# Optimization experiments

Measured on AMD Instinct MI355X. Metric: run time of the kernel, lower is better.

Reference implementation:

```python
import jax, jax.numpy as jnp
import numpy as np

NUM_ATOMS = 4_000_000
NUM_TYPES = 11

def setup_inputs() -> dict:
    key = jax.random.key(0)
    k1, k2 = jax.random.split(key)
    input_coords = jax.random.normal(k1, (3 * NUM_ATOMS,), dtype=jnp.float32)
    atom_types = jax.random.randint(k2, (NUM_ATOMS,), 0, NUM_TYPES, dtype=jnp.int64)
    return {"input_coords": input_coords, "atom_types": atom_types, "num_atom_types": NUM_TYPES}

def reference(input_coords, atom_types, num_atom_types):
    # counts per atom type  [T]
    counts = jnp.bincount(atom_types, length=num_atom_types).astype(jnp.int32)
    # exclusive prefix sum -> bucket offsets  [T]
    offsets = (jnp.cumsum(counts) - counts).astype(jnp.int32)
    # stable sort by type reproduces the C++ bucket fill order:
    # atoms of the same type keep their original relative order.
    perm = jnp.argsort(atom_types, stable=True)  # [N] source index for each output slot
    coords3 = input_coords.reshape(-1, 3)        # [N,3]
    typed_coords = coords3[perm].reshape(-1)     # [3N] type-grouped flat coords
    return typed_coords, counts, offsets
```

## Files before the change

### kernel.cpp

```cpp
#include <hip/hip_runtime.h>

#define NTYPES 11
#define BLOCK  256
#define ITEMS  16
#define CHUNK  (BLOCK * ITEMS)

__global__ __launch_bounds__(BLOCK) void hist_kernel(
    const int* __restrict__ types, int N, int B, int* __restrict__ bc) {
  __shared__ int shCnt[NTYPES];
  const int tid = threadIdx.x;
  const int b = blockIdx.x;
  if (tid < NTYPES) shCnt[tid] = 0;
  __syncthreads();

  const int run = b * CHUNK + tid * ITEMS;
  int cnt[NTYPES];
#pragma unroll
  for (int t = 0; t < NTYPES; ++t) cnt[t] = 0;

  if (run < N) {
    const int* p = types + run;
    int ty[ITEMS];
#pragma unroll
    for (int k = 0; k < ITEMS; ++k) ty[k] = __builtin_nontemporal_load(p + k);
#pragma unroll
    for (int k = 0; k < ITEMS; ++k) {
#pragma unroll
      for (int t = 0; t < NTYPES; ++t) cnt[t] += (ty[k] == t) ? 1 : 0;
    }
  }

  const int lane = tid & 63;
#pragma unroll
  for (int t = 0; t < NTYPES; ++t) {
    int v = cnt[t];
    for (int o = 32; o >= 1; o >>= 1) v += __shfl_down(v, o);
    if (lane == 0) atomicAdd(&shCnt[t], v);
  }
  __syncthreads();
  if (tid < NTYPES) bc[tid * B + b] = shCnt[tid];
}

__global__ __launch_bounds__(NTYPES * 64) void scan_kernel(
    const int* __restrict__ bc, int B, int* __restrict__ scanOut,
    int* __restrict__ offs, float* __restrict__ outTail) {
  __shared__ int totals[NTYPES];
  const int lane = threadIdx.x & 63;
  const int t = threadIdx.x >> 6;

  int carry = 0;
#pragma unroll
  for (int cchunk = 0; cchunk < 16; ++cchunk) {
    const int idx = cchunk * 64 + lane;
    const int x = (idx < B) ? bc[t * B + idx] : 0;
    int incl = x;
#pragma unroll
    for (int o = 1; o < 64; o <<= 1) {
      int v = __shfl_up(incl, o);
      if (lane >= o) incl += v;
    }
    incl += carry;
    if (idx < B) scanOut[t * B + idx] = incl - x;
    carry = __shfl(incl, 63);
    if (cchunk * 64 + 64 >= B && cchunk * 64 < B) break;
  }
  if (lane == 0) totals[t] = carry;
  __syncthreads();

  if (threadIdx.x == 0) {
    int off = 0;
    for (int u = 0; u < NTYPES; ++u) {
      const int c = totals[u];
      offs[u] = off;
      outTail[u] = (float)c;
      outTail[NTYPES + u] = (float)off;
      off += c;
    }
  }
}

__global__ __launch_bounds__(BLOCK) void scatter_kernel(
    const float* __restrict__ coords, const int* __restrict__ types,
    const int* __restrict__ scanOut, const int* __restrict__ offs, int N,
    int B, float* __restrict__ out) {
  __shared__ float shC[CHUNK * 3];
  __shared__ int wtot[NTYPES][4];
  __shared__ int shOff[NTYPES + 1];
  __shared__ int shDelta[NTYPES];

  const int tid = threadIdx.x;
  const int b = blockIdx.x;
  const int lane = tid & 63;
  const int wave = tid >> 6;
  const int run = b * CHUNK + tid * ITEMS;
  const bool active = (run < N);

  int ty[ITEMS];
  int cnt[NTYPES];
#pragma unroll
  for (int t = 0; t < NTYPES; ++t) cnt[t] = 0;
#pragma unroll
  for (int k = 0; k < ITEMS; ++k) ty[k] = -1;

  float c[ITEMS * 3];
  if (active) {
    const int* p = types + run;
#pragma unroll
    for (int k = 0; k < ITEMS; ++k) ty[k] = __builtin_nontemporal_load(p + k);
    const float* cp = coords + (size_t)run * 3;
#pragma unroll
    for (int q = 0; q < ITEMS * 3; ++q)
      c[q] = __builtin_nontemporal_load(cp + q);
#pragma unroll
    for (int k = 0; k < ITEMS; ++k) {
#pragma unroll
      for (int t = 0; t < NTYPES; ++t) cnt[t] += (ty[k] == t) ? 1 : 0;
    }
  }

  int rank[NTYPES];
#pragma unroll
  for (int t = 0; t < NTYPES; ++t) {
    int incl = cnt[t];
#pragma unroll
    for (int o = 1; o < 64; o <<= 1) {
      int v = __shfl_up(incl, o);
      if (lane >= o) incl += v;
    }
    if (lane == 63) wtot[t][wave] = incl;
    rank[t] = incl - cnt[t];
  }
  __syncthreads();

  if (tid < NTYPES) {
    int loc = 0;
    for (int u = 0; u < tid; ++u)
      loc += wtot[u][0] + wtot[u][1] + wtot[u][2] + wtot[u][3];
    shOff[tid] = loc;
    shDelta[tid] = 3 * (offs[tid] + scanOut[tid * B + b] - loc);
    if (tid == NTYPES - 1) {
      shOff[NTYPES] =
          loc + wtot[tid][0] + wtot[tid][1] + wtot[tid][2] + wtot[tid][3];
    }
  }
  __syncthreads();

#pragma unroll
  for (int t = 0; t < NTYPES; ++t) {
    int wb = 0;
#pragma unroll
    for (int w = 0; w < 3; ++w) wb += (w < wave) ? wtot[t][w] : 0;
    rank[t] += wb + shOff[t];
  }

  if (active) {
#pragma unroll
    for (int k = 0; k < ITEMS; ++k) {
      const int t0 = ty[k];
      int slot = 0;
#pragma unroll
      for (int t = 0; t < NTYPES; ++t) {
        if (t0 == t) {
          slot = rank[t];
          rank[t] += 1;
        }
      }
      shC[3 * slot + 0] = c[3 * k + 0];
      shC[3 * slot + 1] = c[3 * k + 1];
      shC[3 * slot + 2] = c[3 * k + 2];
    }
  }
  __syncthreads();

  const int total = shOff[NTYPES];
  int offr[NTYPES];
  int dlt[NTYPES];
#pragma unroll
  for (int t = 0; t < NTYPES; ++t) {
    offr[t] = shOff[t];
    dlt[t] = shDelta[t];
  }
#pragma unroll
  for (int k = 0; k < ITEMS; ++k) {
    const int s = k * BLOCK + tid;
    if (s < total) {
      int d = dlt[0];
#pragma unroll
      for (int t = 1; t < NTYPES; ++t) d = (s >= offr[t]) ? dlt[t] : d;
      const int src = 3 * s;
      out[src + d + 0] = shC[src + 0];
      out[src + d + 1] = shC[src + 1];
      out[src + d + 2] = shC[src + 2];
    }
  }
}

extern "C" void kernel_launch(void* const* d_in, const int* in_sizes, int n_in,
                              void* d_out, int out_size, void* d_ws,
                              size_t ws_size, hipStream_t stream) {
  const float* coords = (const float*)d_in[0];
  const int* types = (const int*)d_in[1];
  const int N = in_sizes[1];
  const int B = (N + CHUNK - 1) / CHUNK;

  int* bc = (int*)d_ws;
  int* scanOut = bc + NTYPES * B;
  int* offs = scanOut + NTYPES * B;
  float* out = (float*)d_out;
  float* outTail = out + (size_t)3 * N;

  hist_kernel<<<B, BLOCK, 0, stream>>>(types, N, B, bc);
  scan_kernel<<<1, NTYPES * 64, 0, stream>>>(bc, B, scanOut, offs, outTail);
  scatter_kernel<<<B, BLOCK, 0, stream>>>(coords, types, scanOut, offs, N, B,
                                          out);
}
```

Measured before the change: 164.6 us.

## Halve items per thread, vectorize type/coord loads, preload scan inputs

Cuts ITEMS from 16 to 8, doubling the block count and shrinking shared memory per block, which should raise occupancy in the scatter kernel. Type and coordinate loads become int4/float4 vector loads instead of scalar nontemporal loads. The scan kernel now loads all per-block counts into registers up front (MAXCH=32 chunks) before the serial scan, so memory latency is not exposed on every chunk. The scan works only while B fits in 32*64 blocks, and the vector loads rely on 16-byte alignment of each thread's slice.

```diff
diff --git a/kernel.cpp b/kernel.cpp
--- a/kernel.cpp
+++ b/kernel.cpp
@@ -2,8 +2,9 @@
 
 #define NTYPES 11
 #define BLOCK  256
-#define ITEMS  16
+#define ITEMS  8
 #define CHUNK  (BLOCK * ITEMS)
+#define MAXCH  32
 
 __global__ __launch_bounds__(BLOCK) void hist_kernel(
     const int* __restrict__ types, int N, int B, int* __restrict__ bc) {
@@ -19,10 +20,9 @@
   for (int t = 0; t < NTYPES; ++t) cnt[t] = 0;
 
   if (run < N) {
-    const int* p = types + run;
-    int ty[ITEMS];
-#pragma unroll
-    for (int k = 0; k < ITEMS; ++k) ty[k] = __builtin_nontemporal_load(p + k);
+    const int4* p = (const int4*)(types + run);
+    int4 a0 = p[0], a1 = p[1];
+    int ty[ITEMS] = {a0.x, a0.y, a0.z, a0.w, a1.x, a1.y, a1.z, a1.w};
 #pragma unroll
     for (int k = 0; k < ITEMS; ++k) {
 #pragma unroll
@@ -47,22 +47,29 @@
   __shared__ int totals[NTYPES];
   const int lane = threadIdx.x & 63;
   const int t = threadIdx.x >> 6;
+  const int nch = (B + 63) >> 6;
+
+  int x[MAXCH];
+#pragma unroll
+  for (int c = 0; c < MAXCH; ++c) {
+    const int idx = c * 64 + lane;
+    x[c] = (c < nch && idx < B) ? bc[t * B + idx] : 0;
+  }
 
   int carry = 0;
 #pragma unroll
-  for (int cchunk = 0; cchunk < 16; ++cchunk) {
-    const int idx = cchunk * 64 + lane;
-    const int x = (idx < B) ? bc[t * B + idx] : 0;
-    int incl = x;
+  for (int c = 0; c < MAXCH; ++c) {
+    if (c >= nch) break;
+    int incl = x[c];
 #pragma unroll
     for (int o = 1; o < 64; o <<= 1) {
       int v = __shfl_up(incl, o);
       if (lane >= o) incl += v;
     }
     incl += carry;
-    if (idx < B) scanOut[t * B + idx] = incl - x;
+    const int idx = c * 64 + lane;
+    if (idx < B) scanOut[t * B + idx] = incl - x[c];
     carry = __shfl(incl, 63);
-    if (cchunk * 64 + 64 >= B && cchunk * 64 < B) break;
   }
   if (lane == 0) totals[t] = carry;
   __syncthreads();
@@ -104,13 +111,20 @@
 
   float c[ITEMS * 3];
   if (active) {
-    const int* p = types + run;
-#pragma unroll
-    for (int k = 0; k < ITEMS; ++k) ty[k] = __builtin_nontemporal_load(p + k);
-    const float* cp = coords + (size_t)run * 3;
-#pragma unroll
-    for (int q = 0; q < ITEMS * 3; ++q)
-      c[q] = __builtin_nontemporal_load(cp + q);
+    const int4* p = (const int4*)(types + run);
+    int4 a0 = p[0], a1 = p[1];
+    int tt[ITEMS] = {a0.x, a0.y, a0.z, a0.w, a1.x, a1.y, a1.z, a1.w};
+#pragma unroll
+    for (int k = 0; k < ITEMS; ++k) ty[k] = tt[k];
+    const float4* cp = (const float4*)(coords + (size_t)run * 3);
+#pragma unroll
+    for (int q = 0; q < (ITEMS * 3) / 4; ++q) {
+      float4 v = cp[q];
+      c[4 * q + 0] = v.x;
+      c[4 * q + 1] = v.y;
+      c[4 * q + 2] = v.z;
+      c[4 * q + 3] = v.w;
+    }
 #pragma unroll
     for (int k = 0; k < ITEMS; ++k) {
 #pragma unroll
```

After: 134.0 us. 1.23x faster.
